# Kernel optimization log

Hardware: AMD Instinct MI355X
Metric: run time of the kernel (lower is better)

Reference implementation:

```python
import jax, jax.numpy as jnp
import numpy as np

BATCH, SEQ_L, H, N = 16, 2048, 512, 64
DT_MIN, DT_MAX = 1e-3, 1e-1


def setup_inputs() -> dict:
    key = jax.random.key(0)
    ks = jax.random.split(key, 6)
    u = jax.random.normal(ks[0], (BATCH, SEQ_L, H), dtype=jnp.float32)
    # S4D diagonal init: stable real part, linearly spaced imaginary frequencies
    Lambda_real = -0.5 * jnp.ones((N,), dtype=jnp.float32)
    Lambda_imag = jnp.pi * jnp.arange(N, dtype=jnp.float32)
    B_real = jax.random.normal(ks[1], (H, N), dtype=jnp.float32) * (N ** -0.5)
    B_imag = jnp.zeros((H, N), dtype=jnp.float32)
    C_real = jax.random.normal(ks[2], (H, N), dtype=jnp.float32) * 0.5
    C_imag = jax.random.normal(ks[3], (H, N), dtype=jnp.float32) * 0.5
    log_dt = (jax.random.uniform(ks[4], (H,), dtype=jnp.float32)
              * (np.float32(np.log(DT_MAX)) - np.float32(np.log(DT_MIN)))
              + np.float32(np.log(DT_MIN)))
    D = jax.random.normal(ks[5], (H,), dtype=jnp.float32) * 0.01
    return {"u": u, "Lambda_real": Lambda_real, "Lambda_imag": Lambda_imag,
            "B_real": B_real, "B_imag": B_imag, "C_real": C_real,
            "C_imag": C_imag, "log_dt": log_dt, "D": D}


def reference(u, Lambda_real, Lambda_imag, B_real, B_imag, C_real, C_imag, log_dt, D):
    # u: (B, L, H)
    Lseq = u.shape[1]
    Lam = Lambda_real + 1j * Lambda_imag            # (N,)
    Bc = B_real + 1j * B_imag                        # (H, N)
    Cc = C_real + 1j * C_imag                        # (H, N)
    dt = jnp.exp(log_dt)                             # (H,)

    # ZOH discretization (matches step(): Ab = exp(dt*Lam), Bb = B*(Ab-1)/(Lam+eps))
    dtA = dt[:, None] * Lam[None, :]                 # (H, N)
    Ab = jnp.exp(dtA)
    Bb = Bc * (Ab - 1.0) / (Lam[None, :] + 1e-8)

    # Vandermonde over all channels at once: V[h,n,l] = exp(dt_h * Lam_n * l)
    ell = jnp.arange(Lseq, dtype=jnp.float32)
    V = jnp.exp(dtA[:, :, None] * ell[None, None, :])  # (H, N, L) complex
    K = jnp.einsum('hn,hnl->hl', Cc * Bb, V).real       # (H, L) real kernel

    # Causal FFT convolution along time
    x = jnp.swapaxes(u, -1, -2)                      # (B, H, L)
    nfft = 2 * Lseq
    Xf = jnp.fft.rfft(x, n=nfft)                     # (B, H, nfft/2+1)
    Kf = jnp.fft.rfft(K, n=nfft)                     # (H, nfft/2+1)
    y = jnp.fft.irfft(Xf * Kf[None], n=nfft)[..., :Lseq]

    y = y + x * D[None, :, None]                     # skip connection
    return jnp.swapaxes(y, -1, -2)                   # (B, L, H)
```

## Files before the change

kernel.cpp:

```cpp
#include <hip/hip_runtime.h>
#include <hip/hip_bf16.h>


#define BSZ 16
#define LSEQ 2048
#define HCH 512
#define NST 64
#define NF 4096

__device__ __forceinline__ int WD(int i) { return 2 * i + ((i >> 4) << 1); }

__device__ __forceinline__ float2 cadd(float2 a, float2 b) { return make_float2(a.x + b.x, a.y + b.y); }
__device__ __forceinline__ float2 csub(float2 a, float2 b) { return make_float2(a.x - b.x, a.y - b.y); }
__device__ __forceinline__ float2 cmul(float2 a, float c, float s) {
    return make_float2(a.x * c - a.y * s, a.x * s + a.y * c);
}
__device__ __forceinline__ float2 cmul2(float2 a, float2 b) {
    return make_float2(a.x * b.x - a.y * b.y, a.x * b.y + a.y * b.x);
}

__device__ __forceinline__ void sincos_red(float a, float* s, float* c) {
    double ad = (double)a;
    double q = rint(ad * 0.15915494309189535);
    float r = (float)(ad - q * 6.283185307179586);
    __sincosf(r, s, c);
}

template <bool INV>
__device__ __forceinline__ void dft8_tail(float2 t0, float2 t1, float2 t2, float2 t3,
                                          float2 t4, float2 t5, float2 t6, float2 t7,
                                          float2& A0, float2& A1, float2& A2, float2& A3,
                                          float2& A4, float2& A5, float2& A6, float2& A7)
{
    const float S = 0.70710678118654752f;
    float2 u0 = cadd(t0, t2), u2 = csub(t0, t2);
    float2 u1 = cadd(t1, t3), u3 = csub(t1, t3);
    A0 = cadd(u0, u1); A4 = csub(u0, u1);
    if constexpr (!INV) {
        A2 = make_float2(u2.x + u3.y, u2.y - u3.x);
        A6 = make_float2(u2.x - u3.y, u2.y + u3.x);
    } else {
        A2 = make_float2(u2.x - u3.y, u2.y + u3.x);
        A6 = make_float2(u2.x + u3.y, u2.y - u3.x);
    }
    float2 b0 = t4, b1, b2, b3;
    if constexpr (!INV) {
        b1 = make_float2(S * (t5.x + t5.y), S * (t5.y - t5.x));
        b2 = make_float2(t6.y, -t6.x);
        b3 = make_float2(S * (t7.y - t7.x), -S * (t7.x + t7.y));
    } else {
        b1 = make_float2(S * (t5.x - t5.y), S * (t5.y + t5.x));
        b2 = make_float2(-t6.y, t6.x);
        b3 = make_float2(-S * (t7.x + t7.y), S * (t7.x - t7.y));
    }
    float2 v0 = cadd(b0, b2), v2 = csub(b0, b2);
    float2 v1 = cadd(b1, b3), v3 = csub(b1, b3);
    A1 = cadd(v0, v1); A5 = csub(v0, v1);
    if constexpr (!INV) {
        A3 = make_float2(v2.x + v3.y, v2.y - v3.x);
        A7 = make_float2(v2.x - v3.y, v2.y + v3.x);
    } else {
        A3 = make_float2(v2.x - v3.y, v2.y + v3.x);
        A7 = make_float2(v2.x + v3.y, v2.y - v3.x);
    }
}

template <int SIDX, bool INV, bool HALF, int NT>
__device__ __forceinline__ void fft8_stage(float* z, int t)
{
    constexpr int lgQ = 9 - 3 * SIDX;
    constexpr int Q = 1 << lgQ;
    constexpr int ITERS = 512 / NT;
    const float asc = -1.5339807878856412e-3f * (float)(1 << (3 * SIDX));
#pragma unroll
    for (int it = 0; it < ITERS; ++it) {
        const int bb = t + NT * it;
        const int j = bb & (Q - 1);
        const int base = ((bb >> lgQ) << (lgQ + 3)) + j;
        float s1, c1;
        __sincosf(asc * (float)j, &s1, &c1);
        if constexpr (INV) s1 = -s1;
        const float c2 = c1 * c1 - s1 * s1, s2 = 2.f * c1 * s1;
        const float c3 = c1 * c2 - s1 * s2, s3 = c1 * s2 + s1 * c2;
        const float c4 = c2 * c2 - s2 * s2, s4 = 2.f * c2 * s2;
        const float c5 = c2 * c3 - s2 * s3, s5 = c2 * s3 + s2 * c3;
        const float c6 = c3 * c3 - s3 * s3, s6 = 2.f * c3 * s3;
        const float c7 = c3 * c4 - s3 * s4, s7 = c3 * s4 + s3 * c4;
        float2 a0 = *(float2*)&z[WD(base + 0 * Q)];
        float2 a1 = *(float2*)&z[WD(base + 1 * Q)];
        float2 a2 = *(float2*)&z[WD(base + 2 * Q)];
        float2 a3 = *(float2*)&z[WD(base + 3 * Q)];
        float2 a4, a5, a6, a7;
        if constexpr (!(HALF && !INV)) {
            a4 = *(float2*)&z[WD(base + 4 * Q)];
            a5 = *(float2*)&z[WD(base + 5 * Q)];
            a6 = *(float2*)&z[WD(base + 6 * Q)];
            a7 = *(float2*)&z[WD(base + 7 * Q)];
        }
        if constexpr (INV) {
            a1 = cmul(a1, c1, s1); a2 = cmul(a2, c2, s2); a3 = cmul(a3, c3, s3);
            a4 = cmul(a4, c4, s4); a5 = cmul(a5, c5, s5); a6 = cmul(a6, c6, s6);
            a7 = cmul(a7, c7, s7);
        }
        float2 t0, t1, t2, t3, t4, t5, t6, t7;
        if constexpr (HALF && !INV) {
            t0 = a0; t4 = a0; t1 = a1; t5 = a1; t2 = a2; t6 = a2; t3 = a3; t7 = a3;
        } else {
            t0 = cadd(a0, a4); t4 = csub(a0, a4);
            t1 = cadd(a1, a5); t5 = csub(a1, a5);
            t2 = cadd(a2, a6); t6 = csub(a2, a6);
            t3 = cadd(a3, a7); t7 = csub(a3, a7);
        }
        float2 A0, A1, A2, A3, A4, A5, A6, A7;
        dft8_tail<INV>(t0, t1, t2, t3, t4, t5, t6, t7, A0, A1, A2, A3, A4, A5, A6, A7);
        if constexpr (!INV) {
            A1 = cmul(A1, c1, s1); A2 = cmul(A2, c2, s2); A3 = cmul(A3, c3, s3);
            A4 = cmul(A4, c4, s4); A5 = cmul(A5, c5, s5); A6 = cmul(A6, c6, s6);
            A7 = cmul(A7, c7, s7);
        }
        *(float2*)&z[WD(base + 0 * Q)] = A0;
        *(float2*)&z[WD(base + 1 * Q)] = A1;
        *(float2*)&z[WD(base + 2 * Q)] = A2;
        *(float2*)&z[WD(base + 3 * Q)] = A3;
        if constexpr (!(HALF && INV)) {
            *(float2*)&z[WD(base + 4 * Q)] = A4;
            *(float2*)&z[WD(base + 5 * Q)] = A5;
            *(float2*)&z[WD(base + 6 * Q)] = A6;
            *(float2*)&z[WD(base + 7 * Q)] = A7;
        }
    }
}

template <int NT>
__device__ __forceinline__ void mid_stage(float* z, const float2* __restrict__ kf, int t)
{
    constexpr int ITERS = 512 / NT;
#pragma unroll
    for (int it = 0; it < ITERS; ++it) {
        const int bb = t + NT * it;
        const int base = bb * 8;
        float2 a[8];
#pragma unroll
        for (int r = 0; r < 8; ++r) a[r] = *(float2*)&z[WD(base + r)];
        float2 t0 = cadd(a[0], a[4]), t4 = csub(a[0], a[4]);
        float2 t1 = cadd(a[1], a[5]), t5 = csub(a[1], a[5]);
        float2 t2 = cadd(a[2], a[6]), t6 = csub(a[2], a[6]);
        float2 t3 = cadd(a[3], a[7]), t7 = csub(a[3], a[7]);
        float2 A0, A1, A2, A3, A4, A5, A6, A7;
        dft8_tail<false>(t0, t1, t2, t3, t4, t5, t6, t7, A0, A1, A2, A3, A4, A5, A6, A7);
        const float2* kp = kf + base;
        A0 = cmul2(A0, kp[0]); A1 = cmul2(A1, kp[1]);
        A2 = cmul2(A2, kp[2]); A3 = cmul2(A3, kp[3]);
        A4 = cmul2(A4, kp[4]); A5 = cmul2(A5, kp[5]);
        A6 = cmul2(A6, kp[6]); A7 = cmul2(A7, kp[7]);
        t0 = cadd(A0, A4); t4 = csub(A0, A4);
        t1 = cadd(A1, A5); t5 = csub(A1, A5);
        t2 = cadd(A2, A6); t6 = csub(A2, A6);
        t3 = cadd(A3, A7); t7 = csub(A3, A7);
        float2 X0, X1, X2, X3, X4, X5, X6, X7;
        dft8_tail<true>(t0, t1, t2, t3, t4, t5, t6, t7, X0, X1, X2, X3, X4, X5, X6, X7);
        *(float2*)&z[WD(base + 0)] = X0;
        *(float2*)&z[WD(base + 1)] = X1;
        *(float2*)&z[WD(base + 2)] = X2;
        *(float2*)&z[WD(base + 3)] = X3;
        *(float2*)&z[WD(base + 4)] = X4;
        *(float2*)&z[WD(base + 5)] = X5;
        *(float2*)&z[WD(base + 6)] = X6;
        *(float2*)&z[WD(base + 7)] = X7;
    }
}

__global__ __launch_bounds__(512, 4) void k_kfft(const float* __restrict__ lam_r,
                                                 const float* __restrict__ lam_i,
                                                 const float* __restrict__ Br,
                                                 const float* __restrict__ Bi,
                                                 const float* __restrict__ Cr,
                                                 const float* __restrict__ Ci,
                                                 const float* __restrict__ log_dt,
                                                 float* __restrict__ gKf)
{
    const int h = blockIdx.x;
    const int t = threadIdx.x;
    __shared__ float z[8704];
    __shared__ float sWr[NST], sWi[NST], sAr[NST], sAi[NST], sDr[NST], sDi[NST];

    if (t < NST) {
        const int n = t;
        float lr = lam_r[n], li = lam_i[n];
        float dt = __expf(log_dt[h]);
        float dar = dt * lr;
        float dai = dt * li;
        float e = __expf(dar);
        float sn, cs; sincos_red(dai, &sn, &cs);
        float Ar = e * cs, Ai = e * sn;
        float nr = Ar - 1.0f, ni = Ai;
        float br = Br[h * NST + n], bi = Bi[h * NST + n];
        float tr = br * nr - bi * ni;
        float ti = br * ni + bi * nr;
        float dr = lr + 1e-8f, di = li;
        float den = dr * dr + di * di;
        float bbr = (tr * dr + ti * di) / den;
        float bbi = (ti * dr - tr * di) / den;
        float cr = Cr[h * NST + n], ci = Ci[h * NST + n];
        sWr[n] = cr * bbr - ci * bbi;
        sWi[n] = cr * bbi + ci * bbr;
        sAr[n] = Ar; sAi[n] = Ai;
        sDr[n] = dar; sDi[n] = dai;
    }
    __syncthreads();

    const int l0 = t * 4;
    float acc[4];
#pragma unroll
    for (int k = 0; k < 4; ++k) acc[k] = 0.0f;
    const float fl0 = (float)l0;
    for (int n = 0; n < NST; ++n) {
        float dar = sDr[n], dai = sDi[n];
        float ang = dai * fl0;
        float sn, cs; sincos_red(ang, &sn, &cs);
        float e = __expf(dar * fl0);
        float pr = e * cs, pi = e * sn;
        float Ar = sAr[n], Ai = sAi[n];
        float wr = sWr[n], wi = sWi[n];
#pragma unroll
        for (int k = 0; k < 4; ++k) {
            acc[k] += wr * pr - wi * pi;
            float npr = pr * Ar - pi * Ai;
            pi = pr * Ai + pi * Ar;
            pr = npr;
        }
    }
#pragma unroll
    for (int k = 0; k < 4; ++k)
        *(float2*)&z[WD(l0 + k)] = make_float2(acc[k], 0.0f);
    __syncthreads();

    fft8_stage<0, false, true , 512>(z, t); __syncthreads();
    fft8_stage<1, false, false, 512>(z, t); __syncthreads();
    fft8_stage<2, false, false, 512>(z, t); __syncthreads();
    fft8_stage<3, false, false, 512>(z, t); __syncthreads();

    float2* out = (float2*)gKf + (size_t)h * NF;
#pragma unroll
    for (int i = 0; i < 8; ++i) {
        int idx = t + 512 * i;
        out[idx] = *(float2*)&z[WD(idx)];
    }
}

__global__ __launch_bounds__(256) void k_transpose_fwd(const float* __restrict__ in,
                                                       float* __restrict__ out)
{
    __shared__ float tile[64][65];
    const int b  = blockIdx.z;
    const int lt = blockIdx.x * 64;
    const int ht = blockIdx.y * 64;
    const int tx = threadIdx.x;
    const int ty = threadIdx.y;
    const float* inb = in + (size_t)b * LSEQ * HCH;
    float* outb = out + (size_t)b * HCH * LSEQ;
#pragma unroll
    for (int i = 0; i < 4; ++i) {
        int r = ty + 16 * i;
        float4 v = *(const float4*)&inb[(size_t)(lt + r) * HCH + ht + 4 * tx];
        tile[r][4 * tx + 0] = v.x;
        tile[r][4 * tx + 1] = v.y;
        tile[r][4 * tx + 2] = v.z;
        tile[r][4 * tx + 3] = v.w;
    }
    __syncthreads();
#pragma unroll
    for (int i = 0; i < 4; ++i) {
        int rp = ty + 16 * i;
        float4 o = make_float4(tile[4 * tx + 0][rp], tile[4 * tx + 1][rp],
                               tile[4 * tx + 2][rp], tile[4 * tx + 3][rp]);
        *(float4*)&outb[(size_t)(ht + rp) * LSEQ + lt + 4 * tx] = o;
    }
}

__global__ __launch_bounds__(256) void k_transpose_bwd(const float* __restrict__ in,
                                                       float* __restrict__ out)
{
    __shared__ float tile[64][65];
    const int b  = blockIdx.z;
    const int lt = blockIdx.x * 64;
    const int ht = blockIdx.y * 64;
    const int tx = threadIdx.x;
    const int ty = threadIdx.y;
    const float* inb = in + (size_t)b * HCH * LSEQ;
    float* outb = out + (size_t)b * LSEQ * HCH;
#pragma unroll
    for (int i = 0; i < 4; ++i) {
        int r = ty + 16 * i;
        float4 v = *(const float4*)&inb[(size_t)(ht + r) * LSEQ + lt + 4 * tx];
        tile[r][4 * tx + 0] = v.x;
        tile[r][4 * tx + 1] = v.y;
        tile[r][4 * tx + 2] = v.z;
        tile[r][4 * tx + 3] = v.w;
    }
    __syncthreads();
#pragma unroll
    for (int i = 0; i < 4; ++i) {
        int rp = ty + 16 * i;
        float4 o = make_float4(tile[4 * tx + 0][rp], tile[4 * tx + 1][rp],
                               tile[4 * tx + 2][rp], tile[4 * tx + 3][rp]);
        *(float4*)&outb[(size_t)(lt + rp) * HCH + ht + 4 * tx] = o;
    }
}

__global__ __launch_bounds__(512, 4) void k_fftconv(float* __restrict__ gut,
                                                    const float* __restrict__ gKf,
                                                    const float* __restrict__ gD)
{
    const int bid = blockIdx.x;
    const int b = bid >> 9;
    const int h = bid & (HCH - 1);
    const int t = threadIdx.x;
    __shared__ float z[8704];

    float* row0 = gut + ((size_t)(b * HCH) + h) * LSEQ;
    float* row1 = gut + ((size_t)((b + 8) * HCH) + h) * LSEQ;

    float4 u0k = ((const float4*)row0)[t];
    float4 u1k = ((const float4*)row1)[t];
    {
        int l = 4 * t;
        *(float2*)&z[WD(l + 0)] = make_float2(u0k.x, u1k.x);
        *(float2*)&z[WD(l + 1)] = make_float2(u0k.y, u1k.y);
        *(float2*)&z[WD(l + 2)] = make_float2(u0k.z, u1k.z);
        *(float2*)&z[WD(l + 3)] = make_float2(u0k.w, u1k.w);
    }
    __syncthreads();

    fft8_stage<0, false, true , 512>(z, t); __syncthreads();
    fft8_stage<1, false, false, 512>(z, t); __syncthreads();
    fft8_stage<2, false, false, 512>(z, t); __syncthreads();
    mid_stage<512>(z, (const float2*)gKf + (size_t)h * NF, t); __syncthreads();
    fft8_stage<2, true, false, 512>(z, t); __syncthreads();
    fft8_stage<1, true, false, 512>(z, t); __syncthreads();
    fft8_stage<0, true, true , 512>(z, t); __syncthreads();

    const float sc = 1.0f / 4096.0f;
    const float Dh = gD[h];
    {
        int l = 4 * t;
        float2 z0 = *(float2*)&z[WD(l + 0)];
        float2 z1 = *(float2*)&z[WD(l + 1)];
        float2 z2 = *(float2*)&z[WD(l + 2)];
        float2 z3 = *(float2*)&z[WD(l + 3)];
        float4 o0 = make_float4(z0.x * sc + Dh * u0k.x, z1.x * sc + Dh * u0k.y,
                                z2.x * sc + Dh * u0k.z, z3.x * sc + Dh * u0k.w);
        float4 o1 = make_float4(z0.y * sc + Dh * u1k.x, z1.y * sc + Dh * u1k.y,
                                z2.y * sc + Dh * u1k.z, z3.y * sc + Dh * u1k.w);
        ((float4*)row0)[t] = o0;
        ((float4*)row1)[t] = o1;
    }
}

extern "C" void kernel_launch(void* const* d_in, const int* in_sizes, int n_in,
                              void* d_out, int out_size, void* d_ws, size_t ws_size,
                              hipStream_t stream)
{
    const float* u      = (const float*)d_in[0];
    const float* lam_r  = (const float*)d_in[1];
    const float* lam_i  = (const float*)d_in[2];
    const float* Br     = (const float*)d_in[3];
    const float* Bi     = (const float*)d_in[4];
    const float* Cr     = (const float*)d_in[5];
    const float* Ci     = (const float*)d_in[6];
    const float* log_dt = (const float*)d_in[7];
    const float* Dv     = (const float*)d_in[8];

    float* gut = (float*)d_ws;
    float* gKf = (float*)d_out;

    k_kfft<<<HCH, 512, 0, stream>>>(lam_r, lam_i, Br, Bi, Cr, Ci, log_dt, gKf);
    k_transpose_fwd<<<dim3(LSEQ / 64, HCH / 64, BSZ), dim3(16, 16, 1), 0, stream>>>(u, gut);
    k_fftconv<<<BSZ / 2 * HCH, 512, 0, stream>>>(gut, gKf, Dv);
    k_transpose_bwd<<<dim3(LSEQ / 64, HCH / 64, BSZ), dim3(16, 16, 1), 0, stream>>>(gut, (float*)d_out);
}
```

Baseline: 238.2 us.

## Split kernel generation from its FFT and co-schedule FFT with input transpose

The Vandermonde kernel evaluation moves into its own light kernel with 2x more blocks of 256 threads and no large LDS buffer, so occupancy should be higher for that compute-heavy step. The kernel FFT and the forward transpose of u are merged into one launch, with block ranges dispatched by block index, so the few FFT blocks overlap with the memory-bound transpose. This adds a workspace round trip for the time-domain kernel and gives the transpose tiles 512-thread blocks with the larger LDS footprint.

```diff
diff --git a/kernel.cpp b/kernel.cpp
--- a/kernel.cpp
+++ b/kernel.cpp
@@ -170,18 +170,18 @@
     }
 }
 
-__global__ __launch_bounds__(512, 4) void k_kfft(const float* __restrict__ lam_r,
-                                                 const float* __restrict__ lam_i,
-                                                 const float* __restrict__ Br,
-                                                 const float* __restrict__ Bi,
-                                                 const float* __restrict__ Cr,
-                                                 const float* __restrict__ Ci,
-                                                 const float* __restrict__ log_dt,
-                                                 float* __restrict__ gKf)
-{
-    const int h = blockIdx.x;
+__global__ __launch_bounds__(256) void k_kgen(const float* __restrict__ lam_r,
+                                              const float* __restrict__ lam_i,
+                                              const float* __restrict__ Br,
+                                              const float* __restrict__ Bi,
+                                              const float* __restrict__ Cr,
+                                              const float* __restrict__ Ci,
+                                              const float* __restrict__ log_dt,
+                                              float* __restrict__ gKt)
+{
+    const int h = blockIdx.x >> 1;
+    const int half = blockIdx.x & 1;
     const int t = threadIdx.x;
-    __shared__ float z[8704];
     __shared__ float sWr[NST], sWi[NST], sAr[NST], sAi[NST], sDr[NST], sDi[NST];
 
     if (t < NST) {
@@ -209,10 +209,8 @@
     }
     __syncthreads();
 
-    const int l0 = t * 4;
-    float acc[4];
-#pragma unroll
-    for (int k = 0; k < 4; ++k) acc[k] = 0.0f;
+    const int l0 = half * 1024 + 4 * t;
+    float acc[4] = {0.f, 0.f, 0.f, 0.f};
     const float fl0 = (float)l0;
     for (int n = 0; n < NST; ++n) {
         float dar = sDr[n], dai = sDi[n];
@@ -230,51 +228,64 @@
             pr = npr;
         }
     }
-#pragma unroll
-    for (int k = 0; k < 4; ++k)
-        *(float2*)&z[WD(l0 + k)] = make_float2(acc[k], 0.0f);
-    __syncthreads();
-
-    fft8_stage<0, false, true , 512>(z, t); __syncthreads();
-    fft8_stage<1, false, false, 512>(z, t); __syncthreads();
-    fft8_stage<2, false, false, 512>(z, t); __syncthreads();
-    fft8_stage<3, false, false, 512>(z, t); __syncthreads();
-
-    float2* out = (float2*)gKf + (size_t)h * NF;
-#pragma unroll
-    for (int i = 0; i < 8; ++i) {
-        int idx = t + 512 * i;
-        out[idx] = *(float2*)&z[WD(idx)];
-    }
-}
-
-__global__ __launch_bounds__(256) void k_transpose_fwd(const float* __restrict__ in,
-                                                       float* __restrict__ out)
-{
-    __shared__ float tile[64][65];
-    const int b  = blockIdx.z;
-    const int lt = blockIdx.x * 64;
-    const int ht = blockIdx.y * 64;
-    const int tx = threadIdx.x;
-    const int ty = threadIdx.y;
-    const float* inb = in + (size_t)b * LSEQ * HCH;
-    float* outb = out + (size_t)b * HCH * LSEQ;
-#pragma unroll
-    for (int i = 0; i < 4; ++i) {
-        int r = ty + 16 * i;
-        float4 v = *(const float4*)&inb[(size_t)(lt + r) * HCH + ht + 4 * tx];
-        tile[r][4 * tx + 0] = v.x;
-        tile[r][4 * tx + 1] = v.y;
-        tile[r][4 * tx + 2] = v.z;
-        tile[r][4 * tx + 3] = v.w;
-    }
-    __syncthreads();
-#pragma unroll
-    for (int i = 0; i < 4; ++i) {
-        int rp = ty + 16 * i;
-        float4 o = make_float4(tile[4 * tx + 0][rp], tile[4 * tx + 1][rp],
-                               tile[4 * tx + 2][rp], tile[4 * tx + 3][rp]);
-        *(float4*)&outb[(size_t)(ht + rp) * LSEQ + lt + 4 * tx] = o;
+    *(float4*)&gKt[(size_t)h * LSEQ + l0] = make_float4(acc[0], acc[1], acc[2], acc[3]);
+}
+
+__global__ __launch_bounds__(512) void k_fused(const float* __restrict__ gKt,
+                                               float* __restrict__ gKf,
+                                               const float* __restrict__ u,
+                                               float* __restrict__ gut)
+{
+    const int bid = blockIdx.x;
+    const int t = threadIdx.x;
+    __shared__ float lds[8704];
+
+    if (bid < HCH) {
+        const int h = bid;
+        float4 kv = ((const float4*)(gKt + (size_t)h * LSEQ))[t];
+        int l = 4 * t;
+        *(float2*)&lds[WD(l + 0)] = make_float2(kv.x, 0.f);
+        *(float2*)&lds[WD(l + 1)] = make_float2(kv.y, 0.f);
+        *(float2*)&lds[WD(l + 2)] = make_float2(kv.z, 0.f);
+        *(float2*)&lds[WD(l + 3)] = make_float2(kv.w, 0.f);
+        __syncthreads();
+        fft8_stage<0, false, true , 512>(lds, t); __syncthreads();
+        fft8_stage<1, false, false, 512>(lds, t); __syncthreads();
+        fft8_stage<2, false, false, 512>(lds, t); __syncthreads();
+        fft8_stage<3, false, false, 512>(lds, t); __syncthreads();
+        float2* out = (float2*)gKf + (size_t)h * NF;
+#pragma unroll
+        for (int i = 0; i < 8; ++i) {
+            int idx = t + 512 * i;
+            out[idx] = *(float2*)&lds[WD(idx)];
+        }
+    } else {
+        float (*tile)[65] = (float (*)[65])lds;
+        const int tid2 = bid - HCH;
+        const int b  = tid2 >> 8;
+        const int ht = ((tid2 >> 5) & 7) * 64;
+        const int lt = (tid2 & 31) * 64;
+        const int tx = t & 15;
+        const int ty = t >> 4;
+        const float* inb = u + (size_t)b * LSEQ * HCH;
+        float* outb = gut + (size_t)b * HCH * LSEQ;
+#pragma unroll
+        for (int i = 0; i < 2; ++i) {
+            int r = ty + 32 * i;
+            float4 v = *(const float4*)&inb[(size_t)(lt + r) * HCH + ht + 4 * tx];
+            tile[r][4 * tx + 0] = v.x;
+            tile[r][4 * tx + 1] = v.y;
+            tile[r][4 * tx + 2] = v.z;
+            tile[r][4 * tx + 3] = v.w;
+        }
+        __syncthreads();
+#pragma unroll
+        for (int i = 0; i < 2; ++i) {
+            int rp = ty + 32 * i;
+            float4 o = make_float4(tile[4 * tx + 0][rp], tile[4 * tx + 1][rp],
+                                   tile[4 * tx + 2][rp], tile[4 * tx + 3][rp]);
+            *(float4*)&outb[(size_t)(ht + rp) * LSEQ + lt + 4 * tx] = o;
+        }
     }
 }
 
@@ -372,10 +383,11 @@
     const float* Dv     = (const float*)d_in[8];
 
     float* gut = (float*)d_ws;
+    float* gKt = (float*)d_ws + (size_t)BSZ * HCH * LSEQ;
     float* gKf = (float*)d_out;
 
-    k_kfft<<<HCH, 512, 0, stream>>>(lam_r, lam_i, Br, Bi, Cr, Ci, log_dt, gKf);
-    k_transpose_fwd<<<dim3(LSEQ / 64, HCH / 64, BSZ), dim3(16, 16, 1), 0, stream>>>(u, gut);
+    k_kgen<<<2 * HCH, 256, 0, stream>>>(lam_r, lam_i, Br, Bi, Cr, Ci, log_dt, gKt);
+    k_fused<<<HCH + 4096, 512, 0, stream>>>(gKt, gKf, u, gut);
     k_fftconv<<<BSZ / 2 * HCH, 512, 0, stream>>>(gut, gKf, Dv);
     k_transpose_bwd<<<dim3(LSEQ / 64, HCH / 64, BSZ), dim3(16, 16, 1), 0, stream>>>(gut, (float*)d_out);
 }
```

After: 229.1 us. -3.8%, faster.
